# Kernel optimization log

Hardware: AMD Instinct MI355X
Metric: run time of the kernel (lower is better)

Reference implementation:

```python
import jax, jax.numpy as jnp
import numpy as np

B, L, D = 8, 2048, 256


def setup_inputs() -> dict:
    key = jax.random.key(0)
    k1, k2, k3, k4, k5, k6 = jax.random.split(key, 6)
    c1 = jax.random.normal(k1, (B, L, D), dtype=jnp.float32)
    c2 = jax.random.normal(k2, (B, L, D), dtype=jnp.float32)
    c_mask = jnp.zeros((B, L), dtype=bool)  # True = padded position
    # FusionLayer params: linear_f: (4D -> D), linear_g: (4D -> 1)
    s = 1.0 / np.sqrt(4 * D)
    W_f = jax.random.uniform(k3, (4 * D, D), dtype=jnp.float32, minval=-s, maxval=s)
    b_f = jax.random.uniform(k4, (D,), dtype=jnp.float32, minval=-s, maxval=s)
    W_g = jax.random.uniform(k5, (4 * D, 1), dtype=jnp.float32, minval=-s, maxval=s)
    b_g = jax.random.uniform(k6, (1,), dtype=jnp.float32, minval=-s, maxval=s)
    return {"c1": c1, "c2": c2, "c_mask": c_mask, "W_f": W_f, "b_f": b_f,
            "W_g": W_g, "b_g": b_g, "flag": 1}


def reference(c1, c2, c_mask, W_f, b_f, W_g, b_g, flag):
    # flag == 1 -> forward_fuse path
    # AttentionScore default (correlation_func=1): scores[b,i,j] = c2[b,i] . c1[b,j]
    scores = jnp.einsum('bid,bjd->bij', c2, c1)  # [B, L, L]
    neg_inf = jnp.array(-jnp.inf, dtype=scores.dtype)
    diag = jnp.eye(scores.shape[1], dtype=bool)[None]        # [1, L, L]
    scores = jnp.where(diag, neg_inf, scores)                 # mask self-attention diag
    scores = jnp.where(c_mask[:, None, :], neg_inf, scores)   # mask padded keys
    alpha = jax.nn.softmax(scores, axis=2)                    # [B, L, L]
    aug_c2 = jnp.einsum('bij,bjd->bid', alpha, c1)            # [B, L, D]
    # FusionLayer: z = [x, y, x*y, x-y]; out = g*tanh(Wf z) + (1-g)*x
    z = jnp.concatenate([c2, aug_c2, c2 * aug_c2, c2 - aug_c2], axis=2)  # [B, L, 4D]
    gated = jax.nn.sigmoid(z @ W_g + b_g)                     # [B, L, 1]
    fusion = jnp.tanh(z @ W_f + b_f)                          # [B, L, D]
    return gated * fusion + (1.0 - gated) * c2
```

## Files before the change

kernel.cpp:

```cpp
#include <hip/hip_runtime.h>
#include <math.h>

#define BB 8
#define LL 2048
#define DD 256

typedef float  f4_t __attribute__((ext_vector_type(4)));
typedef short  s8_t __attribute__((ext_vector_type(8)));

union S8U { s8_t v; unsigned u[4]; };

__device__ __forceinline__ unsigned bitsf(float x){ union{float f; unsigned u;} c; c.f=x; return c.u; }
__device__ __forceinline__ float fbits(unsigned u){ union{float f; unsigned u;} c; c.u=u; return c.f; }
__device__ __forceinline__ unsigned pkhi(float a, float b){ return (bitsf(a)>>16) | (bitsf(b)&0xffff0000u); }
__device__ __forceinline__ unsigned pkrn(float a, float b){
    unsigned ua = bitsf(a) + 0x8000u, ub = bitsf(b) + 0x8000u;
    return (ua>>16) | (ub&0xffff0000u);
}
__device__ __forceinline__ short rnb(float a){ return (short)((bitsf(a) + 0x8000u) >> 16); }

__device__ __forceinline__ int vslot(int e){ return ((e>>2)&3)*8 + ((e>>4)<<2) + (e&3); }

__global__ __launch_bounds__(512,1)
void attn_kernel(const float* __restrict__ c1, const float* __restrict__ c2,
                 const unsigned char* __restrict__ cmask,
                 float* __restrict__ o0, float* __restrict__ o1,
                 float* __restrict__ mlp,
                 const float* __restrict__ Wf, const float* __restrict__ Wg,
                 unsigned* __restrict__ Whi, unsigned* __restrict__ Wlo,
                 float* __restrict__ gw,
                 int klen, int split, int nattn)
{
    __shared__ short    KhiS[2][32*264];
    __shared__ unsigned VpS [2][256*20];

    if ((int)blockIdx.x >= nattn) {
        const int pb  = blockIdx.x - nattn;
        const int ptid = threadIdx.x;
        if (pb == 192) {
            if (ptid < 256) {
#pragma unroll
                for (int i = 0; i < 3; ++i) {
                    float v = (i == 0) ? (Wg[ptid] + Wg[768 + ptid])
                            : (i == 1) ? (Wg[256 + ptid] - Wg[768 + ptid])
                                       :  Wg[512 + ptid];
                    gw[i*256 + ptid] = v;
                }
            }
            return;
        }
        int t    = pb*512 + ptid;
        int p    = t & 3;
        int lane = (t >> 2) & 63;
        int nt   = (t >> 8) & 15;
        int g2   = t >> 12;
        int seg  = g2 % 3;
        int kc   = g2 / 3;
        int kl   = kc*32 + (lane >> 4)*8 + 2*p;
        int n    = nt*16 + (lane & 15);
        float v0, v1;
        if (seg == 0) {
            v0 = Wf[(size_t)kl*DD + n]       + Wf[(size_t)(768 + kl)*DD + n];
            v1 = Wf[(size_t)(kl + 1)*DD + n] + Wf[(size_t)(769 + kl)*DD + n];
        } else if (seg == 1) {
            v0 = Wf[(size_t)(256 + kl)*DD + n] - Wf[(size_t)(768 + kl)*DD + n];
            v1 = Wf[(size_t)(257 + kl)*DD + n] - Wf[(size_t)(769 + kl)*DD + n];
        } else {
            v0 = Wf[(size_t)(512 + kl)*DD + n];
            v1 = Wf[(size_t)(513 + kl)*DD + n];
        }
        Whi[t] = pkhi(v0, v1);
        float l0 = v0 - fbits(bitsf(v0) & 0xffff0000u);
        float l1 = v1 - fbits(bitsf(v1) & 0xffff0000u);
        Wlo[t] = pkrn(l0, l1);
        return;
    }

    const int tid  = threadIdx.x;
    const int lane = tid & 63;
    const int w    = tid >> 6;
    const int il   = lane & 15;
    const int quad = lane >> 4;
    const int col  = tid & 255;
    const int hr   = (tid >> 8) * 16;
    const int xv   = (col >> 3) & 3;

    const int blk  = blockIdx.x;
    const int bb   = blk & 7;
    const int qb   = (blk >> 3) & 15;
    const int half = split ? ((blk >> 7) & 1) : 0;
    const int kb   = half * klen;

    float* ob = half ? o1 : o0;

    const float* c1b = c1 + (size_t)bb * LL * DD;
    const float* c2b = c2 + (size_t)bb * LL * DD;
    const unsigned char* mb = cmask + (size_t)bb * LL;

    const int q0w = qb*128 + w*16;

    s8_t qh[8], ql[8];
    {
        const float* qp = c2b + (size_t)(q0w + il)*DD + quad*8;
#pragma unroll
        for (int kd = 0; kd < 8; ++kd) {
            float4 x0 = *(const float4*)(qp + kd*32);
            float4 x1 = *(const float4*)(qp + kd*32 + 4);
            float e[8] = {x0.x,x0.y,x0.z,x0.w,x1.x,x1.y,x1.z,x1.w};
            S8U h, l;
#pragma unroll
            for (int p2 = 0; p2 < 4; ++p2) {
                float a = e[2*p2], b = e[2*p2+1];
                h.u[p2] = pkhi(a, b);
                float alo = a - fbits(bitsf(a)&0xffff0000u);
                float blo = b - fbits(bitsf(b)&0xffff0000u);
                l.u[p2] = pkhi(alo, blo);
            }
            qh[kd] = h.v; ql[kd] = l.v;
        }
    }

    f4_t o[16];
#pragma unroll
    for (int n = 0; n < 16; ++n) o[n] = (f4_t)0.0f;
    float m_s = -INFINITY;
    float l_s = 0.f;

    const int NT = klen >> 5;
    float g[16];

#define STAGE_WRITE(KH, VP) do { \
    _Pragma("unroll") \
    for (int e_ = 0; e_ < 16; ++e_) \
        (KH)[(hr + e_)*264 + col] = rnb(g[e_]); \
    _Pragma("unroll") \
    for (int e_ = 0; e_ < 16; e_ += 2) { \
        const int s_ = vslot(hr + e_) >> 1; \
        (VP)[col*20 + (((s_ >> 2) ^ xv) << 2) + (s_ & 3)] = pkrn(g[e_], g[e_+1]); \
    } \
} while (0)

#pragma unroll
    for (int e = 0; e < 16; ++e) g[e] = c1b[(size_t)(kb + hr + e)*DD + col];
    STAGE_WRITE(KhiS[0], VpS[0]);
    __syncthreads();

    int cur = 0;
    for (int kt = 0; kt < NT; ++kt) {
        const int k0 = kt << 5;
        if (kt + 1 < NT) {
#pragma unroll
            for (int e = 0; e < 16; ++e)
                g[e] = c1b[(size_t)(kb + k0 + 32 + hr + e)*DD + col];
        }

        const short*    Khi = KhiS[cur];
        const unsigned* Vp  = VpS[cur];

        f4_t acc[2];
        acc[0] = (f4_t)0.0f;
        acc[1] = (f4_t)0.0f;

#pragma unroll
        for (int kd = 0; kd < 8; ++kd) {
            s8_t ah0 = *(const s8_t*)&Khi[(il     )*264 + kd*32 + quad*8];
            s8_t ah1 = *(const s8_t*)&Khi[(16 + il)*264 + kd*32 + quad*8];
            acc[0] = __builtin_amdgcn_mfma_f32_16x16x32_bf16(ah0, qh[kd], acc[0], 0,0,0);
            acc[1] = __builtin_amdgcn_mfma_f32_16x16x32_bf16(ah1, qh[kd], acc[1], 0,0,0);
            acc[0] = __builtin_amdgcn_mfma_f32_16x16x32_bf16(ah0, ql[kd], acc[0], 0,0,0);
            acc[1] = __builtin_amdgcn_mfma_f32_16x16x32_bf16(ah1, ql[kd], acc[1], 0,0,0);
        }

        unsigned mu[2];
#pragma unroll
        for (int mj = 0; mj < 2; ++mj)
            mu[mj] = *(const unsigned*)(mb + kb + k0 + 16*mj + 4*quad);

        const int ig = q0w + il;
        float tm = -INFINITY;
        f4_t p[2];
#pragma unroll
        for (int mj = 0; mj < 2; ++mj) {
#pragma unroll
            for (int b = 0; b < 4; ++b) {
                int jg = kb + k0 + 16*mj + 4*quad + b;
                float s = acc[mj][b];
                bool dead = (((mu[mj] >> (8*b)) & 0xff) != 0) || (jg == ig);
                s = dead ? -INFINITY : s;
                p[mj][b] = s;
                tm = fmaxf(tm, s);
            }
        }
        tm = fmaxf(tm, __shfl_xor(tm, 16, 64));
        tm = fmaxf(tm, __shfl_xor(tm, 32, 64));
        const bool stable = __all(tm <= m_s);
        const float mn = stable ? m_s : fmaxf(m_s, tm);
        float rs = 0.f;
#pragma unroll
        for (int mj = 0; mj < 2; ++mj) {
#pragma unroll
            for (int b = 0; b < 4; ++b) {
                float pe = __expf(p[mj][b] - mn);
                p[mj][b] = pe;
                rs += pe;
            }
        }
        rs += __shfl_xor(rs, 16, 64);
        rs += __shfl_xor(rs, 32, 64);
        if (!stable) {
            float al = __expf(m_s - mn);
            l_s = l_s*al + rs;
            m_s = mn;
            float am[4];
#pragma unroll
            for (int b = 0; b < 4; ++b) am[b] = __shfl(al, 4*quad + b, 64);
#pragma unroll
            for (int n = 0; n < 16; ++n) {
#pragma unroll
                for (int b = 0; b < 4; ++b) o[n][b] *= am[b];
            }
        } else {
            l_s += rs;
        }

        s8_t ap;
        {
            S8U a;
            a.u[0] = pkrn(p[0][0], p[0][1]);
            a.u[1] = pkrn(p[0][2], p[0][3]);
            a.u[2] = pkrn(p[1][0], p[1][1]);
            a.u[3] = pkrn(p[1][2], p[1][3]);
            ap = a.v;
        }
#pragma unroll
        for (int n = 0; n < 16; ++n) {
            const int vr = 16*n + il;
            s8_t bv = *(const s8_t*)(Vp + vr*20 + ((quad ^ ((vr >> 3) & 3)) << 2));
            o[n] = __builtin_amdgcn_mfma_f32_16x16x32_bf16(ap, bv, o[n], 0,0,0);
        }

        if (kt + 1 < NT) {
            short*    KhiN = KhiS[cur^1];
            unsigned* VpN  = VpS[cur^1];
            STAGE_WRITE(KhiN, VpN);
        }
        __syncthreads();
        cur ^= 1;
    }
#undef STAGE_WRITE

    const int rbq = bb*LL + q0w;
    if (split) {
        const int rbase = rbq + 4*quad;
#pragma unroll
        for (int n = 0; n < 16; ++n) {
            const int d = 16*n + il;
#pragma unroll
            for (int b = 0; b < 4; ++b)
                ob[(size_t)(rbase + b)*DD + d] = o[n][b];
        }
        if (lane < 16) {
            int r = rbq + lane;
            *(float2*)(&mlp[((size_t)half*16384 + r)*2]) = make_float2(m_s, l_s);
        }
    } else {
        float invl[4];
#pragma unroll
        for (int b = 0; b < 4; ++b) invl[b] = 1.0f / __shfl(l_s, 4*quad + b, 64);
        const int rbase = rbq + 4*quad;
#pragma unroll
        for (int n = 0; n < 16; ++n) {
            const int d = 16*n + il;
#pragma unroll
            for (int b = 0; b < 4; ++b)
                ob[(size_t)(rbase + b)*DD + d] = o[n][b] * invl[b];
        }
    }
}

__global__ __launch_bounds__(512,1)
void fusion_mfma(const float* __restrict__ c2,
                 const float* __restrict__ P0, const float* __restrict__ P1,
                 const float* __restrict__ mlp,
                 const unsigned* __restrict__ Whi, const unsigned* __restrict__ Wlo,
                 const float* __restrict__ gw, const float* __restrict__ bg,
                 const float* __restrict__ bf, float* __restrict__ out, int ns)
{
    __shared__ float    gwL[768];
    __shared__ unsigned zA[2][64*20];
    __shared__ unsigned zB[2][64*20];
    __shared__ unsigned zC[2][64*20];
    __shared__ float    gpart[64][8];
    __shared__ float    gv[64];

    const int tid  = threadIdx.x;
    const int lane = tid & 63;
    const int w    = tid >> 6;
    const int il   = lane & 15;
    const int quad = lane >> 4;
    const int srow = tid >> 3;
    const int scg  = tid & 7;
    const size_t row0 = (size_t)blockIdx.x * 64;

    const float* c2b = c2 + row0*DD;
    const float* P0b = P0 + row0*DD;
    const float* P1b = P1 + row0*DD;

    for (int i = tid; i < 768; i += 512) gwL[i] = gw[i];

    float ca0 = 1.f, ca1 = 0.f;
    if (ns == 2) {
        const size_t r = row0 + srow;
        float m0 = mlp[r*2],             l0 = mlp[r*2 + 1];
        float m1 = mlp[(16384 + r)*2],   l1 = mlp[(16384 + r)*2 + 1];
        float M  = fmaxf(m0, m1);
        float a0 = __expf(m0 - M), a1 = __expf(m1 - M);
        float inv = 1.0f / (a0*l0 + a1*l1);
        ca0 = a0*inv; ca1 = a1*inv;
    }
    __syncthreads();

    float gatep = 0.f;
    float4 pr4; f4_t u4;

#define FLOAD(kc_) do { \
    const int off_ = srow*DD + (kc_)*32 + scg*4; \
    pr4 = *(const float4*)(c2b + off_); \
    u4  = *(const f4_t*)(P0b + off_); \
    if (ns == 2) { \
        f4_t v4_ = *(const f4_t*)(P1b + off_); \
        u4 = u4*ca0 + v4_*ca1; \
    } \
} while (0)

#define FCONV(buf_, kc_) do { \
    const int co_ = (kc_)*32 + scg*4; \
    float ea0_ = pr4.x, ea1_ = pr4.y, ea2_ = pr4.z, ea3_ = pr4.w; \
    float d0_ = ea0_*u4[0], d1_ = ea1_*u4[1], d2_ = ea2_*u4[2], d3_ = ea3_*u4[3]; \
    gatep += ea0_*gwL[co_+0] + u4[0]*gwL[256+co_+0] + d0_*gwL[512+co_+0] \
           + ea1_*gwL[co_+1] + u4[1]*gwL[256+co_+1] + d1_*gwL[512+co_+1] \
           + ea2_*gwL[co_+2] + u4[2]*gwL[256+co_+2] + d2_*gwL[512+co_+2] \
           + ea3_*gwL[co_+3] + u4[3]*gwL[256+co_+3] + d3_*gwL[512+co_+3]; \
    const int zi_ = srow*20 + scg*2; \
    *(uint2*)&zA[buf_][zi_] = make_uint2(pkrn(ea0_, ea1_), pkrn(ea2_, ea3_)); \
    *(uint2*)&zB[buf_][zi_] = make_uint2(pkrn(u4[0], u4[1]), pkrn(u4[2], u4[3])); \
    *(uint2*)&zC[buf_][zi_] = make_uint2(pkrn(d0_, d1_),   pkrn(d2_, d3_)); \
} while (0)

    f4_t acc[4][2];
#pragma unroll
    for (int mt = 0; mt < 4; ++mt)
#pragma unroll
        for (int nt = 0; nt < 2; ++nt) acc[mt][nt] = (f4_t)0.0f;

    FLOAD(0); FCONV(0, 0);
    __syncthreads();

    int cur = 0;
    for (int kc = 0; kc < 8; ++kc) {
        if (kc + 1 < 8) FLOAD(kc + 1);

        s8_t fa[4], fb[4], fc[4];
#pragma unroll
        for (int mt = 0; mt < 4; ++mt) {
            const int fi = (16*mt + il)*20 + quad*4;
            fa[mt] = *(const s8_t*)&zA[cur][fi];
            fb[mt] = *(const s8_t*)&zB[cur][fi];
            fc[mt] = *(const s8_t*)&zC[cur][fi];
        }
#pragma unroll
        for (int nt = 0; nt < 2; ++nt) {
            const int ntg = w*2 + nt;
            const size_t f0 = ((size_t)((kc*3 + 0)*16 + ntg)*64 + lane)*4;
            const size_t f1 = ((size_t)((kc*3 + 1)*16 + ntg)*64 + lane)*4;
            const size_t f2 = ((size_t)((kc*3 + 2)*16 + ntg)*64 + lane)*4;
            s8_t w0h = *(const s8_t*)(Whi + f0), w0l = *(const s8_t*)(Wlo + f0);
            s8_t w1h = *(const s8_t*)(Whi + f1), w1l = *(const s8_t*)(Wlo + f1);
            s8_t w2h = *(const s8_t*)(Whi + f2), w2l = *(const s8_t*)(Wlo + f2);
#pragma unroll
            for (int mt = 0; mt < 4; ++mt) {
                acc[mt][nt] = __builtin_amdgcn_mfma_f32_16x16x32_bf16(fa[mt], w0h, acc[mt][nt], 0,0,0);
                acc[mt][nt] = __builtin_amdgcn_mfma_f32_16x16x32_bf16(fa[mt], w0l, acc[mt][nt], 0,0,0);
                acc[mt][nt] = __builtin_amdgcn_mfma_f32_16x16x32_bf16(fb[mt], w1h, acc[mt][nt], 0,0,0);
                acc[mt][nt] = __builtin_amdgcn_mfma_f32_16x16x32_bf16(fb[mt], w1l, acc[mt][nt], 0,0,0);
                acc[mt][nt] = __builtin_amdgcn_mfma_f32_16x16x32_bf16(fc[mt], w2h, acc[mt][nt], 0,0,0);
                acc[mt][nt] = __builtin_amdgcn_mfma_f32_16x16x32_bf16(fc[mt], w2l, acc[mt][nt], 0,0,0);
            }
        }

        if (kc + 1 < 8) FCONV(cur ^ 1, kc + 1);
        __syncthreads();
        cur ^= 1;
    }
#undef FLOAD
#undef FCONV

    gpart[srow][scg] = gatep;
    __syncthreads();
    if (tid < 64) {
        float s = 0.f;
#pragma unroll
        for (int cg = 0; cg < 8; ++cg) s += gpart[tid][cg];
        gv[tid] = 1.0f / (1.0f + __expf(-(s + bg[0])));
    }
    __syncthreads();

#pragma unroll
    for (int nt = 0; nt < 2; ++nt) {
        const int col = w*32 + nt*16 + il;
        const float bfv = bf[col];
#pragma unroll
        for (int mt = 0; mt < 4; ++mt) {
#pragma unroll
            for (int b = 0; b < 4; ++b) {
                const int r = 16*mt + 4*quad + b;
                const float g = gv[r];
                const float cc = c2b[(size_t)r*DD + col];
                out[(row0 + r)*DD + col] = g * tanhf(acc[mt][nt][b] + bfv) + (1.f - g) * cc;
            }
        }
    }
}

extern "C" void kernel_launch(void* const* d_in, const int* in_sizes, int n_in,
                              void* d_out, int out_size, void* d_ws, size_t ws_size,
                              hipStream_t stream)
{
    const float* c1 = (const float*)d_in[0];
    const float* c2 = (const float*)d_in[1];
    const unsigned char* cmask = (const unsigned char*)d_in[2];
    const float* Wf = (const float*)d_in[3];
    const float* bf = (const float*)d_in[4];
    const float* Wg = (const float*)d_in[5];
    const float* bg = (const float*)d_in[6];

    const size_t aug_elems   = (size_t)16384 * 256;
    const size_t frag_elems  = (size_t)98304;

    const size_t ml2_elems = (size_t)2 * 16384 * 2;
    const size_t need2     = (2*aug_elems + ml2_elems + aug_elems) * sizeof(float);

    float* wsf = (float*)d_ws;

    if (ws_size >= need2) {
        float* Op0 = wsf;
        float* Op1 = wsf + aug_elems;
        float* mlp = wsf + 2*aug_elems;
        unsigned* Whi = (unsigned*)(wsf + 2*aug_elems + ml2_elems);
        unsigned* Wlo = Whi + frag_elems;
        float*    gw  = (float*)(Wlo + frag_elems);

        attn_kernel<<<dim3(449), dim3(512), 0, stream>>>(c1, c2, cmask,
                                                         Op0, Op1, mlp,
                                                         Wf, Wg, Whi, Wlo, gw,
                                                         1024, 1, 256);
        fusion_mfma<<<dim3(256), dim3(512), 0, stream>>>(c2, Op0, Op1, mlp,
                                                         Whi, Wlo, gw, bg, bf,
                                                         (float*)d_out, 2);
    } else {
        float* aug = wsf;
        unsigned* Whi = (unsigned*)(wsf + aug_elems);
        unsigned* Wlo = Whi + frag_elems;
        float*    gw  = (float*)(Wlo + frag_elems);

        attn_kernel<<<dim3(321), dim3(512), 0, stream>>>(c1, c2, cmask,
                                                         aug, aug, wsf,
                                                         Wf, Wg, Whi, Wlo, gw,
                                                         2048, 0, 128);
        fusion_mfma<<<dim3(256), dim3(512), 0, stream>>>(c2, aug, aug, wsf,
                                                         Whi, Wlo, gw, bg, bf,
                                                         (float*)d_out, 1);
    }
}
```

Baseline: 200.8 us.

## Split fusion into z-prep pack kernel and 512-block MFMA GEMM

```diff
diff --git a/kernel.cpp b/kernel.cpp
--- a/kernel.cpp
+++ b/kernel.cpp
@@ -278,6 +278,135 @@
     }
 }
 
+__global__ __launch_bounds__(256)
+void zprep_kernel(const float* __restrict__ c2,
+                  const float* __restrict__ P0, const float* __restrict__ P1,
+                  const float* __restrict__ mlp, const float* __restrict__ gw,
+                  const float* __restrict__ bg,
+                  unsigned* __restrict__ zG, float* __restrict__ gv, int ns)
+{
+    __shared__ float gwL[768];
+    __shared__ float gpart[32][8];
+
+    const int tid = threadIdx.x;
+    const int sr  = tid >> 3;
+    const int cg  = tid & 7;
+    const size_t row = (size_t)blockIdx.x * 32 + sr;
+    const int rb   = (int)(row >> 6);
+    const int mt   = (int)((row >> 4) & 3);
+    const int il   = (int)(row & 15);
+    const int quad = cg >> 1;
+    const int lane = quad*16 + il;
+    const int hf   = cg & 1;
+
+    const float* c2r = c2 + row*DD;
+    const float* p0r = P0 + row*DD;
+    const float* p1r = P1 + row*DD;
+
+    for (int i = tid; i < 768; i += 256) gwL[i] = gw[i];
+
+    float ca0 = 1.f, ca1 = 0.f;
+    if (ns == 2) {
+        float m0 = mlp[row*2],             l0 = mlp[row*2 + 1];
+        float m1 = mlp[(16384 + row)*2],   l1 = mlp[(16384 + row)*2 + 1];
+        float M  = fmaxf(m0, m1);
+        float a0 = __expf(m0 - M), a1 = __expf(m1 - M);
+        float inv = 1.0f / (a0*l0 + a1*l1);
+        ca0 = a0*inv; ca1 = a1*inv;
+    }
+    __syncthreads();
+
+    float gatep = 0.f;
+#pragma unroll
+    for (int kc = 0; kc < 8; ++kc) {
+        const int co = kc*32 + cg*4;
+        float4 pr4 = *(const float4*)(c2r + co);
+        f4_t   u4  = *(const f4_t*)(p0r + co);
+        if (ns == 2) {
+            f4_t v4 = *(const f4_t*)(p1r + co);
+            u4 = u4*ca0 + v4*ca1;
+        }
+        float ea0 = pr4.x, ea1 = pr4.y, ea2 = pr4.z, ea3 = pr4.w;
+        float d0 = ea0*u4[0], d1 = ea1*u4[1], d2 = ea2*u4[2], d3 = ea3*u4[3];
+        gatep += ea0*gwL[co+0] + u4[0]*gwL[256+co+0] + d0*gwL[512+co+0]
+               + ea1*gwL[co+1] + u4[1]*gwL[256+co+1] + d1*gwL[512+co+1]
+               + ea2*gwL[co+2] + u4[2]*gwL[256+co+2] + d2*gwL[512+co+2]
+               + ea3*gwL[co+3] + u4[3]*gwL[256+co+3] + d3*gwL[512+co+3];
+        const size_t base = ((((size_t)(rb*8 + kc)*3 + 0)*4 + mt)*64 + lane)*4 + hf*2;
+        *(uint2*)&zG[base       ] = make_uint2(pkrn(ea0, ea1), pkrn(ea2, ea3));
+        *(uint2*)&zG[base + 1024] = make_uint2(pkrn(u4[0], u4[1]), pkrn(u4[2], u4[3]));
+        *(uint2*)&zG[base + 2048] = make_uint2(pkrn(d0, d1), pkrn(d2, d3));
+    }
+    gpart[sr][cg] = gatep;
+    __syncthreads();
+    if (tid < 32) {
+        float s = 0.f;
+#pragma unroll
+        for (int c = 0; c < 8; ++c) s += gpart[tid][c];
+        gv[(size_t)blockIdx.x*32 + tid] = 1.0f / (1.0f + __expf(-(s + bg[0])));
+    }
+}
+
+__global__ __launch_bounds__(512,1)
+void fusion_gemm(const float* __restrict__ c2, const unsigned* __restrict__ zG,
+                 const unsigned* __restrict__ Whi, const unsigned* __restrict__ Wlo,
+                 const float* __restrict__ gv, const float* __restrict__ bf,
+                 float* __restrict__ out)
+{
+    const int tid  = threadIdx.x;
+    const int lane = tid & 63;
+    const int w    = tid >> 6;
+    const int il   = lane & 15;
+    const int quad = lane >> 4;
+    const int rb   = blockIdx.x & 255;
+    const int ch   = blockIdx.x >> 8;
+    const size_t row0 = (size_t)rb * 64;
+    const int ntg  = ch*8 + w;
+
+    f4_t acc[4];
+#pragma unroll
+    for (int mt = 0; mt < 4; ++mt) acc[mt] = (f4_t)0.0f;
+
+    for (int kc = 0; kc < 8; ++kc) {
+        s8_t fa[4], fb[4], fc[4];
+#pragma unroll
+        for (int mt = 0; mt < 4; ++mt) {
+            const size_t zi = ((((size_t)(rb*8 + kc)*3 + 0)*4 + mt)*64 + lane)*4;
+            fa[mt] = *(const s8_t*)&zG[zi];
+            fb[mt] = *(const s8_t*)&zG[zi + 1024];
+            fc[mt] = *(const s8_t*)&zG[zi + 2048];
+        }
+        const size_t f0 = ((size_t)((kc*3 + 0)*16 + ntg)*64 + lane)*4;
+        const size_t f1 = ((size_t)((kc*3 + 1)*16 + ntg)*64 + lane)*4;
+        const size_t f2 = ((size_t)((kc*3 + 2)*16 + ntg)*64 + lane)*4;
+        s8_t w0h = *(const s8_t*)(Whi + f0), w0l = *(const s8_t*)(Wlo + f0);
+        s8_t w1h = *(const s8_t*)(Whi + f1), w1l = *(const s8_t*)(Wlo + f1);
+        s8_t w2h = *(const s8_t*)(Whi + f2), w2l = *(const s8_t*)(Wlo + f2);
+#pragma unroll
+        for (int mt = 0; mt < 4; ++mt) {
+            acc[mt] = __builtin_amdgcn_mfma_f32_16x16x32_bf16(fa[mt], w0h, acc[mt], 0,0,0);
+            acc[mt] = __builtin_amdgcn_mfma_f32_16x16x32_bf16(fa[mt], w0l, acc[mt], 0,0,0);
+            acc[mt] = __builtin_amdgcn_mfma_f32_16x16x32_bf16(fb[mt], w1h, acc[mt], 0,0,0);
+            acc[mt] = __builtin_amdgcn_mfma_f32_16x16x32_bf16(fb[mt], w1l, acc[mt], 0,0,0);
+            acc[mt] = __builtin_amdgcn_mfma_f32_16x16x32_bf16(fc[mt], w2h, acc[mt], 0,0,0);
+            acc[mt] = __builtin_amdgcn_mfma_f32_16x16x32_bf16(fc[mt], w2l, acc[mt], 0,0,0);
+        }
+    }
+
+    const int col = ch*128 + w*16 + il;
+    const float bfv = bf[col];
+#pragma unroll
+    for (int mt = 0; mt < 4; ++mt) {
+#pragma unroll
+        for (int b = 0; b < 4; ++b) {
+            const int r = 16*mt + 4*quad + b;
+            const float g = gv[row0 + r];
+            const float cc = c2[(row0 + r)*DD + col];
+            out[(row0 + r)*DD + col] = g * tanhf(acc[mt][b] + bfv) + (1.f - g) * cc;
+        }
+    }
+}
+
 __global__ __launch_bounds__(512,1)
 void fusion_mfma(const float* __restrict__ c2,
                  const float* __restrict__ P0, const float* __restrict__ P1,
@@ -434,29 +563,34 @@
     const float* Wg = (const float*)d_in[5];
     const float* bg = (const float*)d_in[6];
 
-    const size_t aug_elems   = (size_t)16384 * 256;
-    const size_t frag_elems  = (size_t)98304;
-
-    const size_t ml2_elems = (size_t)2 * 16384 * 2;
-    const size_t need2     = (2*aug_elems + ml2_elems + aug_elems) * sizeof(float);
+    const size_t aug_elems  = (size_t)16384 * 256;
+    const size_t frag_elems = (size_t)98304;
+    const size_t ml2_elems  = (size_t)2 * 16384 * 2;
+    const size_t z_elems    = (size_t)6291456;
+
+    const size_t need_new = (aug_elems + ml2_elems + 2*frag_elems + 768
+                             + z_elems + 16384) * sizeof(float);
 
     float* wsf = (float*)d_ws;
 
-    if (ws_size >= need2) {
-        float* Op0 = wsf;
-        float* Op1 = wsf + aug_elems;
-        float* mlp = wsf + 2*aug_elems;
-        unsigned* Whi = (unsigned*)(wsf + 2*aug_elems + ml2_elems);
+    if (ws_size >= need_new) {
+        float*    Op0 = wsf;
+        float*    mlp = wsf + aug_elems;
+        unsigned* Whi = (unsigned*)(mlp + ml2_elems);
         unsigned* Wlo = Whi + frag_elems;
         float*    gw  = (float*)(Wlo + frag_elems);
+        unsigned* zG  = (unsigned*)(gw + 768);
+        float*    gvp = (float*)(zG + z_elems);
+        float*    Op1 = (float*)d_out;
 
         attn_kernel<<<dim3(449), dim3(512), 0, stream>>>(c1, c2, cmask,
                                                          Op0, Op1, mlp,
                                                          Wf, Wg, Whi, Wlo, gw,
                                                          1024, 1, 256);
-        fusion_mfma<<<dim3(256), dim3(512), 0, stream>>>(c2, Op0, Op1, mlp,
-                                                         Whi, Wlo, gw, bg, bf,
-                                                         (float*)d_out, 2);
+        zprep_kernel<<<dim3(512), dim3(256), 0, stream>>>(c2, Op0, Op1, mlp,
+                                                          gw, bg, zG, gvp, 2);
+        fusion_gemm<<<dim3(512), dim3(512), 0, stream>>>(c2, zG, Whi, Wlo,
+                                                         gvp, bf, (float*)d_out);
     } else {
         float* aug = wsf;
         unsigned* Whi = (unsigned*)(wsf + aug_elems);
```

Measured after the change: 207.0 us. 3.1% more time.
